# Kernel tuning notes

Hardware: AMD Instinct MI355X
Metric: run time of the kernel (lower is better)

The kernel has to match this reference:

```python
import jax, jax.numpy as jnp
import numpy as np

IN_FEATURES = 8192
OUT_FEATURES = 28672


def setup_inputs() -> dict:
    key = jax.random.key(0)
    k1, k2, k3 = jax.random.split(key, 3)
    inputs = jax.random.normal(k1, (16, 1, IN_FEATURES), dtype=jnp.float32)
    # int8 quantized weight (stored as int8, values in [-127, 127])
    weight = jax.random.randint(k2, (OUT_FEATURES, IN_FEATURES), -127, 128, dtype=jnp.int8)
    # per-output-channel dequant scale
    weight_scaler = jax.random.uniform(k3, (OUT_FEATURES,), dtype=jnp.float32) * 0.01 + 1e-4
    return {"inputs": inputs, "weight": weight, "weight_scaler": weight_scaler}


def reference(inputs, weight, weight_scaler):
    # F.linear(inputs, weight): [..., in] @ [out, in]^T -> [..., out]
    # int8 weight is promoted to the activation dtype for the matmul,
    # then the per-channel scale is applied to the output.
    w = weight.astype(inputs.dtype)
    out = jnp.einsum('bsi,oi->bso', inputs, w)  # [B, S, out]
    return out * weight_scaler  # broadcast over last (out-channel) dim
```

## Files before the change

### kernel.cpp

```cpp
#include <hip/hip_runtime.h>
#include <hip/hip_bf16.h>
#include <stdint.h>


using f32x4 = __attribute__((ext_vector_type(4))) float;
using s16x8 = __attribute__((ext_vector_type(8))) short;
using i32x4 = __attribute__((ext_vector_type(4))) int;

static constexpr int K      = 8192;
static constexpr int N      = 28672;
static constexpr int NSTEPS = K / 32;
static constexpr int WK     = 512;
static constexpr int NWIN   = K / WK;
static constexpr int WAVES  = 4;
static constexpr int SPW    = (WK / 32) / WAVES;
static constexpr int LPB    = 16384;

__global__ __launch_bounds__(256) void prep_a_kernel(const float* __restrict__ act,
                                                     uint4* __restrict__ afrag) {
  const int t   = blockIdx.x * 256 + threadIdx.x;
  const int kk  = t >> 6;
  const int l   = t & 63;
  const int row = l & 15;
  const int q   = l >> 4;
  const float* src = act + row * K + kk * 32 + q * 8;
  uint d[4];
#pragma unroll
  for (int p = 0; p < 4; ++p) {
    uint u0 = __builtin_bit_cast(uint, src[2 * p]);
    uint u1 = __builtin_bit_cast(uint, src[2 * p + 1]);
    u0 += 0x7fffu + ((u0 >> 16) & 1u);
    u1 += 0x7fffu + ((u1 >> 16) & 1u);
    d[p] = (u0 >> 16) | (u1 & 0xffff0000u);
  }
  afrag[t] = make_uint4(d[0], d[1], d[2], d[3]);
}

__device__ __forceinline__ uint pack_bf16(int a, int b) {
  uint fa = __builtin_bit_cast(uint, (float)a);
  uint fb = __builtin_bit_cast(uint, (float)b);
  return (fa >> 16) | (fb & 0xffff0000u);
}

__global__ __launch_bounds__(256) void wq_linear_kernel(
    const int* __restrict__ wt,
    const uint4* __restrict__ afrag,
    const float* __restrict__ scaler,
    float* __restrict__ out) {
  __shared__ unsigned char lds[2][LPB];
  const int tid = threadIdx.x;
  const int l   = tid & 63;
  const int w   = tid >> 6;
  const int n0  = blockIdx.x << 4;
  const int r   = l & 15;
  const int q   = l >> 4;

  const int lrow = (w << 2) + (l >> 4);
  const int lc   = l & 15;
  const int* grow = wt + (size_t)(n0 + lrow) * K + lc * 4;
  const int wbase = ((lrow << 10) + (lc << 3)) ^ ((lrow & 7) << 4);

  f32x4 acc = {0.f, 0.f, 0.f, 0.f};
  i32x4 st[8];

#pragma unroll
  for (int i = 0; i < 8; ++i) st[i] = *(const i32x4*)(grow + i * 64);
#pragma unroll
  for (int i = 0; i < 8; ++i) {
    uint2 v = {pack_bf16(st[i].x, st[i].y), pack_bf16(st[i].z, st[i].w)};
    *(uint2*)(&lds[0][wbase + i * 128]) = v;
  }
  __syncthreads();

#pragma unroll 1
  for (int m = 0; m < NWIN; ++m) {
    if (m + 1 < NWIN) {
      const int* g = grow + (m + 1) * WK;
#pragma unroll
      for (int i = 0; i < 8; ++i) st[i] = *(const i32x4*)(g + i * 64);
    }

    const unsigned char* buf = lds[m & 1];
#pragma unroll
    for (int s = 0; s < SPW; ++s) {
      const int stp = (w << 2) + s;
      const int kk  = m * (WK / 32) + stp;
      const uint4 av = afrag[(size_t)kk * 64 + l];
      const int rb = ((r << 10) + (stp << 6) + (q << 4)) ^ ((r & 7) << 4);
      const uint4 bv = *(const uint4*)(&buf[rb]);
      s16x8 a = __builtin_bit_cast(s16x8, av);
      s16x8 b = __builtin_bit_cast(s16x8, bv);
      acc = __builtin_amdgcn_mfma_f32_16x16x32_bf16(a, b, acc, 0, 0, 0);
    }

    if (m + 1 < NWIN) {
      unsigned char* dst = lds[(m + 1) & 1];
#pragma unroll
      for (int i = 0; i < 8; ++i) {
        uint2 v = {pack_bf16(st[i].x, st[i].y), pack_bf16(st[i].z, st[i].w)};
        *(uint2*)(&dst[wbase + i * 128]) = v;
      }
    }
    __syncthreads();
  }

  float* red = (float*)&lds[0][0];
#pragma unroll
  for (int i = 0; i < 4; ++i)
    red[w * 256 + ((q << 2) + i) * 16 + r] = acc[i];
  __syncthreads();

  const float sum = red[0 * 256 + tid] + red[1 * 256 + tid] +
                    red[2 * 256 + tid] + red[3 * 256 + tid];
  const int col = tid & 15;
  const int row = tid >> 4;
  out[(size_t)row * N + n0 + col] = sum * scaler[n0 + col];
}

extern "C" void kernel_launch(void* const* d_in, const int* in_sizes, int n_in,
                              void* d_out, int out_size, void* d_ws, size_t ws_size,
                              hipStream_t stream) {
  const float* act    = (const float*)d_in[0];
  const int*   wt     = (const int*)d_in[1];
  const float* scaler = (const float*)d_in[2];
  float*       out    = (float*)d_out;
  uint4*       afrag  = (uint4*)d_ws;

  prep_a_kernel<<<(NSTEPS * 64) / 256, 256, 0, stream>>>(act, afrag);
  wq_linear_kernel<<<N / 16, 256, 0, stream>>>(wt, afrag, scaler, out);
}
```

Before: 191.2 us.

## Deepen weight prefetch to two windows and hoist activation fragment loads

Weight tiles are now prefetched two windows ahead into a second register set, and the pack into LDS for the next window happens before the MFMA loop instead of after it. Activation fragments for a window are loaded into registers at the top of each iteration, and the global weight load pattern changes so each wave reads whole contiguous rows. Launch bounds request four blocks per CU and the main loop is unrolled by two. This is meant to hide more global-memory latency in this bandwidth-bound int8 GEMV, at the cost of higher register pressure that could cause spills or limit occupancy.

```diff
diff --git a/kernel.cpp b/kernel.cpp
--- a/kernel.cpp
+++ b/kernel.cpp
@@ -42,7 +42,7 @@
   return (fa >> 16) | (fb & 0xffff0000u);
 }
 
-__global__ __launch_bounds__(256) void wq_linear_kernel(
+__global__ __launch_bounds__(256, 4) void wq_linear_kernel(
     const int* __restrict__ wt,
     const uint4* __restrict__ afrag,
     const float* __restrict__ scaler,
@@ -55,52 +55,56 @@
   const int r   = l & 15;
   const int q   = l >> 4;
 
-  const int lrow = (w << 2) + (l >> 4);
-  const int lc   = l & 15;
-  const int* grow = wt + (size_t)(n0 + lrow) * K + lc * 4;
-  const int wbase = ((lrow << 10) + (lc << 3)) ^ ((lrow & 7) << 4);
+  const int* gw = wt + (size_t)(n0 + (w << 2)) * K + (l << 2);
+  const int  rowbase = w << 2;
 
+  i32x4 st[8], st2[8];
+  uint4 ag[SPW];
   f32x4 acc = {0.f, 0.f, 0.f, 0.f};
-  i32x4 st[8];
 
-#pragma unroll
-  for (int i = 0; i < 8; ++i) st[i] = *(const i32x4*)(grow + i * 64);
-#pragma unroll
-  for (int i = 0; i < 8; ++i) {
-    uint2 v = {pack_bf16(st[i].x, st[i].y), pack_bf16(st[i].z, st[i].w)};
-    *(uint2*)(&lds[0][wbase + i * 128]) = v;
+#define LOADW(dst, m)                                                      \
+  _Pragma("unroll") for (int j = 0; j < 8; ++j) {                          \
+    const int rr = j >> 1, h = j & 1;                                      \
+    dst[j] = *(const i32x4*)(gw + rr * K + (m) * WK + h * 256);            \
   }
+
+#define PACKW(s, bi)                                                       \
+  _Pragma("unroll") for (int j = 0; j < 8; ++j) {                          \
+    const int rr = j >> 1, h = j & 1;                                      \
+    const int row = rowbase + rr;                                          \
+    const int ad = ((row << 10) + (h << 9) + (l << 3)) ^ ((row & 7) << 4); \
+    uint2 v = {pack_bf16(s[j].x, s[j].y), pack_bf16(s[j].z, s[j].w)};      \
+    *(uint2*)(&lds[bi][ad]) = v;                                           \
+  }
+
+  LOADW(st, 0)
+  PACKW(st, 0)
+  LOADW(st, 1)
   __syncthreads();
 
-#pragma unroll 1
+#pragma unroll 2
   for (int m = 0; m < NWIN; ++m) {
-    if (m + 1 < NWIN) {
-      const int* g = grow + (m + 1) * WK;
 #pragma unroll
-      for (int i = 0; i < 8; ++i) st[i] = *(const i32x4*)(g + i * 64);
-    }
+    for (int s = 0; s < SPW; ++s)
+      ag[s] = afrag[(size_t)((m << 4) + (w << 2) + s) * 64 + l];
+
+    if (m + 2 < NWIN) { LOADW(st2, m + 2) }
+
+    if (m + 1 < NWIN) { PACKW(st, (m + 1) & 1) }
 
     const unsigned char* buf = lds[m & 1];
 #pragma unroll
     for (int s = 0; s < SPW; ++s) {
       const int stp = (w << 2) + s;
-      const int kk  = m * (WK / 32) + stp;
-      const uint4 av = afrag[(size_t)kk * 64 + l];
-      const int rb = ((r << 10) + (stp << 6) + (q << 4)) ^ ((r & 7) << 4);
+      const int rb  = ((r << 10) + (stp << 6) + (q << 4)) ^ ((r & 7) << 4);
       const uint4 bv = *(const uint4*)(&buf[rb]);
-      s16x8 a = __builtin_bit_cast(s16x8, av);
+      s16x8 a = __builtin_bit_cast(s16x8, ag[s]);
       s16x8 b = __builtin_bit_cast(s16x8, bv);
       acc = __builtin_amdgcn_mfma_f32_16x16x32_bf16(a, b, acc, 0, 0, 0);
     }
 
-    if (m + 1 < NWIN) {
-      unsigned char* dst = lds[(m + 1) & 1];
 #pragma unroll
-      for (int i = 0; i < 8; ++i) {
-        uint2 v = {pack_bf16(st[i].x, st[i].y), pack_bf16(st[i].z, st[i].w)};
-        *(uint2*)(&dst[wbase + i * 128]) = v;
-      }
-    }
+    for (int j = 0; j < 8; ++j) st[j] = st2[j];
     __syncthreads();
   }
 
```

After: 196.7 us. +2.9%, slower.

## Split each block's K-window across 16 waves with one MFMA per wave

Applied to the files above, without the earlier changes.

The GEMV block grows from 4 to 16 waves. Each wave now loads and converts one weight row slice per window and issues a single MFMA for its K-step, instead of four MFMAs per wave. The aim is more memory requests in flight per block and less serial work per wave, to hide global-load latency on the weight stream. The cost is a 16-way final reduction through LDS and tighter register limits from the launch bounds.

```diff
diff --git a/kernel.cpp b/kernel.cpp
--- a/kernel.cpp
+++ b/kernel.cpp
@@ -12,9 +12,8 @@
 static constexpr int NSTEPS = K / 32;
 static constexpr int WK     = 512;
 static constexpr int NWIN   = K / WK;
-static constexpr int WAVES  = 4;
-static constexpr int SPW    = (WK / 32) / WAVES;
-static constexpr int LPB    = 16384;
+static constexpr int WAVES  = 16;
+static constexpr int LPB    = 16 * WK * 2;
 
 __global__ __launch_bounds__(256) void prep_a_kernel(const float* __restrict__ act,
                                                      uint4* __restrict__ afrag) {
@@ -42,7 +41,7 @@
   return (fa >> 16) | (fb & 0xffff0000u);
 }
 
-__global__ __launch_bounds__(256) void wq_linear_kernel(
+__global__ __launch_bounds__(1024, 8) void wq_linear_kernel(
     const int* __restrict__ wt,
     const uint4* __restrict__ afrag,
     const float* __restrict__ scaler,
@@ -55,50 +54,43 @@
   const int r   = l & 15;
   const int q   = l >> 4;
 
-  const int lrow = (w << 2) + (l >> 4);
-  const int lc   = l & 15;
-  const int* grow = wt + (size_t)(n0 + lrow) * K + lc * 4;
-  const int wbase = ((lrow << 10) + (lc << 3)) ^ ((lrow & 7) << 4);
+  const int* gw = wt + (size_t)(n0 + w) * K + (l << 2);
 
+  i32x4 st[2];
   f32x4 acc = {0.f, 0.f, 0.f, 0.f};
-  i32x4 st[8];
 
 #pragma unroll
-  for (int i = 0; i < 8; ++i) st[i] = *(const i32x4*)(grow + i * 64);
+  for (int j = 0; j < 2; ++j) st[j] = *(const i32x4*)(gw + (j << 8));
 #pragma unroll
-  for (int i = 0; i < 8; ++i) {
-    uint2 v = {pack_bf16(st[i].x, st[i].y), pack_bf16(st[i].z, st[i].w)};
-    *(uint2*)(&lds[0][wbase + i * 128]) = v;
+  for (int j = 0; j < 2; ++j) {
+    const int ad = ((w << 10) + (j << 9) + (l << 3)) ^ ((w & 7) << 4);
+    uint2 v = {pack_bf16(st[j].x, st[j].y), pack_bf16(st[j].z, st[j].w)};
+    *(uint2*)(&lds[0][ad]) = v;
   }
   __syncthreads();
 
 #pragma unroll 1
   for (int m = 0; m < NWIN; ++m) {
+    const uint4 ag = afrag[(size_t)((m << 4) + w) * 64 + l];
+
     if (m + 1 < NWIN) {
-      const int* g = grow + (m + 1) * WK;
+      const int* g = gw + (m + 1) * WK;
 #pragma unroll
-      for (int i = 0; i < 8; ++i) st[i] = *(const i32x4*)(g + i * 64);
+      for (int j = 0; j < 2; ++j) st[j] = *(const i32x4*)(g + (j << 8));
     }
 
-    const unsigned char* buf = lds[m & 1];
-#pragma unroll
-    for (int s = 0; s < SPW; ++s) {
-      const int stp = (w << 2) + s;
-      const int kk  = m * (WK / 32) + stp;
-      const uint4 av = afrag[(size_t)kk * 64 + l];
-      const int rb = ((r << 10) + (stp << 6) + (q << 4)) ^ ((r & 7) << 4);
-      const uint4 bv = *(const uint4*)(&buf[rb]);
-      s16x8 a = __builtin_bit_cast(s16x8, av);
-      s16x8 b = __builtin_bit_cast(s16x8, bv);
-      acc = __builtin_amdgcn_mfma_f32_16x16x32_bf16(a, b, acc, 0, 0, 0);
-    }
+    const int rb = ((r << 10) + (w << 6) + (q << 4)) ^ ((r & 7) << 4);
+    const uint4 bv = *(const uint4*)(&lds[m & 1][rb]);
+    s16x8 a = __builtin_bit_cast(s16x8, ag);
+    s16x8 b = __builtin_bit_cast(s16x8, bv);
+    acc = __builtin_amdgcn_mfma_f32_16x16x32_bf16(a, b, acc, 0, 0, 0);
 
     if (m + 1 < NWIN) {
-      unsigned char* dst = lds[(m + 1) & 1];
 #pragma unroll
-      for (int i = 0; i < 8; ++i) {
-        uint2 v = {pack_bf16(st[i].x, st[i].y), pack_bf16(st[i].z, st[i].w)};
-        *(uint2*)(&dst[wbase + i * 128]) = v;
+      for (int j = 0; j < 2; ++j) {
+        const int ad = ((w << 10) + (j << 9) + (l << 3)) ^ ((w & 7) << 4);
+        uint2 v = {pack_bf16(st[j].x, st[j].y), pack_bf16(st[j].z, st[j].w)};
+        *(uint2*)(&lds[(m + 1) & 1][ad]) = v;
       }
     }
     __syncthreads();
@@ -110,11 +102,14 @@
     red[w * 256 + ((q << 2) + i) * 16 + r] = acc[i];
   __syncthreads();
 
-  const float sum = red[0 * 256 + tid] + red[1 * 256 + tid] +
-                    red[2 * 256 + tid] + red[3 * 256 + tid];
-  const int col = tid & 15;
-  const int row = tid >> 4;
-  out[(size_t)row * N + n0 + col] = sum * scaler[n0 + col];
+  if (tid < 256) {
+    float sum = 0.f;
+#pragma unroll
+    for (int ww = 0; ww < WAVES; ++ww) sum += red[ww * 256 + tid];
+    const int col = tid & 15;
+    const int row = tid >> 4;
+    out[(size_t)row * N + n0 + col] = sum * scaler[n0 + col];
+  }
 }
 
 extern "C" void kernel_launch(void* const* d_in, const int* in_sizes, int n_in,
@@ -127,5 +122,5 @@
   uint4*       afrag  = (uint4*)d_ws;
 
   prep_a_kernel<<<(NSTEPS * 64) / 256, 256, 0, stream>>>(act, afrag);
-  wq_linear_kernel<<<N / 16, 256, 0, stream>>>(wt, afrag, scaler, out);
+  wq_linear_kernel<<<N / 16, 1024, 0, stream>>>(wt, afrag, scaler, out);
 }
```

Result: slower. 211.6 us (+10.7%).
